# Performance work log

Hardware: AMD Instinct MI355X
Metric: run time of the kernel (lower is better)

## Reference

```python
import jax, jax.numpy as jnp
import numpy as np

BATCH = 2048
OBS_DIM = 48
H0, H1, H2 = 512, 256, 128
ACT_DIM = 12
NUM_TEACHERS = 64


def setup_inputs() -> dict:
    key = jax.random.key(0)
    ks = jax.random.split(key, 10)
    s = lambda fan_in: 1.0 / np.sqrt(fan_in)
    return {
        "obs": jax.random.normal(ks[0], (BATCH, OBS_DIM), dtype=jnp.float32),
        "teacher_indices": jax.random.randint(ks[1], (BATCH,), 0, NUM_TEACHERS),
        "w0": jax.random.normal(ks[2], (NUM_TEACHERS, H0, OBS_DIM), dtype=jnp.float32) * s(OBS_DIM),
        "b0": jax.random.normal(ks[3], (NUM_TEACHERS, H0), dtype=jnp.float32) * s(OBS_DIM),
        "w2": jax.random.normal(ks[4], (NUM_TEACHERS, H1, H0), dtype=jnp.float32) * s(H0),
        "b2": jax.random.normal(ks[5], (NUM_TEACHERS, H1), dtype=jnp.float32) * s(H0),
        "w4": jax.random.normal(ks[6], (NUM_TEACHERS, H2, H1), dtype=jnp.float32) * s(H1),
        "b4": jax.random.normal(ks[7], (NUM_TEACHERS, H2), dtype=jnp.float32) * s(H1),
        "w6": jax.random.normal(ks[8], (NUM_TEACHERS, ACT_DIM, H2), dtype=jnp.float32) * s(H2),
        "b6": jax.random.normal(ks[9], (NUM_TEACHERS, ACT_DIM), dtype=jnp.float32) * s(H2),
    }


def reference(obs, teacher_indices, w0, b0, w2, b2, w4, b4, w6, b6):
    # Per-sample gather of full teacher layer weights, then batched GEMV.
    def layer(x, w, b):
        # x: [B, in]; w[idx]: [B, out, in]; b[idx]: [B, out]
        return jnp.einsum("boi,bi->bo", w[teacher_indices], x) + b[teacher_indices]

    x = jax.nn.elu(layer(obs, w0, b0))
    x = jax.nn.elu(layer(x, w2, b2))
    x = jax.nn.elu(layer(x, w4, b4))
    x = jnp.tanh(layer(x, w6, b6))
    return x
```

## Files before the change

### kernel.cpp

```cpp
#include <hip/hip_runtime.h>

#define BATCH 2048
#define NTEACH 64

typedef __attribute__((ext_vector_type(8))) short short8;
typedef __attribute__((ext_vector_type(4))) float f32x4;

__device__ __forceinline__ unsigned short f2bf(float f) {
    unsigned u = __float_as_uint(f);
    u += 0x7FFFu + ((u >> 16) & 1u);
    return (unsigned short)(u >> 16);
}

__device__ __forceinline__ short8 cvt8(float4 a, float4 b) {
    short8 r;
    r[0] = (short)f2bf(a.x); r[1] = (short)f2bf(a.y);
    r[2] = (short)f2bf(a.z); r[3] = (short)f2bf(a.w);
    r[4] = (short)f2bf(b.x); r[5] = (short)f2bf(b.y);
    r[6] = (short)f2bf(b.z); r[7] = (short)f2bf(b.w);
    return r;
}

__device__ __forceinline__ int2 wave_scan(const int* __restrict__ tidx,
                                          int t, int* ord) {
    const int lane = threadIdx.x & 63;
    int base = 0, lt = 0;
#pragma unroll
    for (int r = 0; r < 32; ++r) {
        int i = r * 64 + lane;
        int v = tidx[i];
        bool f = (v == t);
        lt += (v < t) ? 1 : 0;
        unsigned long long b = __ballot(f);
        if (ord && f) {
            int rank = base + __builtin_popcountll(b & ((1ull << lane) - 1ull));
            ord[rank] = i;
        }
        base += __builtin_popcountll(b);
    }
#pragma unroll
    for (int off = 32; off; off >>= 1) lt += __shfl_down(lt, off);
    lt = __shfl(lt, 0);
    return make_int2(lt, base);
}

__global__ __launch_bounds__(256) void l0_kernel(const float* __restrict__ obs,
                                                 const int* __restrict__ tidx,
                                                 const float* __restrict__ w0,
                                                 const float* __restrict__ b0,
                                                 int* __restrict__ offsets_g,
                                                 int* __restrict__ order_g,
                                                 unsigned short* __restrict__ h0) {
    __shared__ int ord[BATCH];
    const int t = blockIdx.y;
    const int lane = threadIdx.x & 63, wid = threadIdx.x >> 6;
    const int ln = lane & 15, kg = lane >> 4;
    const int nq = wid & 1, mq = wid >> 1;
    const int n0 = blockIdx.x * 32 + nq * 16;

    const float* wr = w0 + ((size_t)t * 512 + n0 + ln) * 48;
    bool wvalid[2];
    float4 wa[2], wb[2];
#pragma unroll
    for (int kt = 0; kt < 2; ++kt) {
        int kb = kt * 32 + kg * 8;
        wvalid[kt] = kb < 48;
        const float* p = wr + (wvalid[kt] ? kb : 0);
        wa[kt] = *(const float4*)p;
        wb[kt] = *(const float4*)(p + 4);
    }
    const float bias = b0[(size_t)t * 512 + n0 + ln];

    int2 sc = wave_scan(tidx, t, ord);
    const int start = sc.x, count = sc.y;

    if (blockIdx.x == 0) {
        if (threadIdx.x == 0) {
            offsets_g[t] = start;
            if (t == 0) offsets_g[NTEACH] = BATCH;
        }
        for (int i = threadIdx.x; i < count; i += 256) order_g[start + i] = ord[i];
    }
    if (count == 0) return;

    short8 bf[2];
#pragma unroll
    for (int kt = 0; kt < 2; ++kt) {
        short8 z = {0, 0, 0, 0, 0, 0, 0, 0};
        bf[kt] = wvalid[kt] ? cvt8(wa[kt], wb[kt]) : z;
    }

    for (int r0 = mq * 16; r0 < count; r0 += 32) {
        int lr = r0 + ln;
        const float* xr = obs + (size_t)ord[lr < count ? lr : 0] * 48;
        short8 af[2];
#pragma unroll
        for (int kt = 0; kt < 2; ++kt) {
            int kb = kt * 32 + kg * 8;
            short8 f8 = {0, 0, 0, 0, 0, 0, 0, 0};
            if (kb < 48)
                f8 = cvt8(*(const float4*)(xr + kb), *(const float4*)(xr + kb + 4));
            af[kt] = f8;
        }
        f32x4 acc = {0.f, 0.f, 0.f, 0.f};
        acc = __builtin_amdgcn_mfma_f32_16x16x32_bf16(af[0], bf[0], acc, 0, 0, 0);
        acc = __builtin_amdgcn_mfma_f32_16x16x32_bf16(af[1], bf[1], acc, 0, 0, 0);
#pragma unroll
        for (int j = 0; j < 4; ++j) {
            int row = r0 + kg * 4 + j;
            if (row < count) {
                float v = acc[j] + bias;
                v = v > 0.f ? v : expm1f(v);
                h0[(size_t)(start + row) * 512 + n0 + ln] = f2bf(v);
            }
        }
    }
}

__global__ __launch_bounds__(256) void l1_kernel(const unsigned short* __restrict__ h0,
                                                 const int* __restrict__ offsets_g,
                                                 const float* __restrict__ w2,
                                                 const float* __restrict__ b2,
                                                 unsigned short* __restrict__ h1) {
    const int t = blockIdx.y;
    const int start = offsets_g[t];
    const int count = offsets_g[t + 1] - start;
    if (count == 0) return;
    const int lane = threadIdx.x & 63, wid = threadIdx.x >> 6;
    const int ln = lane & 15, kg = lane >> 4;
    const int nq = wid & 1, mq = wid >> 1;
    const int n0 = blockIdx.x * 32 + nq * 16;

    const float* wr = w2 + ((size_t)t * 256 + n0 + ln) * 512;
    const float bias = b2[(size_t)t * 256 + n0 + ln];
    short8 bf[16];
#pragma unroll
    for (int g = 0; g < 4; ++g) {
        float4 ta[4], tb[4];
#pragma unroll
        for (int u = 0; u < 4; ++u) {
            int kb = (g * 4 + u) * 32 + kg * 8;
            ta[u] = *(const float4*)(wr + kb);
            tb[u] = *(const float4*)(wr + kb + 4);
        }
#pragma unroll
        for (int u = 0; u < 4; ++u) bf[g * 4 + u] = cvt8(ta[u], tb[u]);
    }

    for (int r0 = mq * 16; r0 < count; r0 += 32) {
        const unsigned short* xr = h0 + (size_t)(start + r0 + ln) * 512 + kg * 8;
        f32x4 acc = {0.f, 0.f, 0.f, 0.f};
#pragma unroll
        for (int k8 = 0; k8 < 16; ++k8)
            acc = __builtin_amdgcn_mfma_f32_16x16x32_bf16(
                *(const short8*)(xr + k8 * 32), bf[k8], acc, 0, 0, 0);
#pragma unroll
        for (int j = 0; j < 4; ++j) {
            int row = r0 + kg * 4 + j;
            if (row < count) {
                float v = acc[j] + bias;
                v = v > 0.f ? v : expm1f(v);
                h1[(size_t)(start + row) * 256 + n0 + ln] = f2bf(v);
            }
        }
    }
}

__global__ __launch_bounds__(256) void l2f_kernel(const unsigned short* __restrict__ h1,
                                                  const int* __restrict__ offsets_g,
                                                  const int* __restrict__ order_g,
                                                  const float* __restrict__ w4,
                                                  const float* __restrict__ b4,
                                                  const float* __restrict__ w6,
                                                  const float* __restrict__ b6,
                                                  float* __restrict__ out) {
    __shared__ char h2b[4096];
    const int t = blockIdx.y;
    const int start = offsets_g[t];
    const int count = offsets_g[t + 1] - start;
    if ((int)blockIdx.x * 16 >= count) return;
    const int lane = threadIdx.x & 63, wid = threadIdx.x >> 6;
    const int ln = lane & 15, kg = lane >> 4;
    const int nq = wid;

    short8 bfA[2][8];
    float biasA[2];
#pragma unroll
    for (int sub = 0; sub < 2; ++sub) {
        const float* wr = w4 + ((size_t)t * 128 + nq * 32 + sub * 16 + ln) * 256;
#pragma unroll
        for (int g = 0; g < 2; ++g) {
            float4 ta[4], tb[4];
#pragma unroll
            for (int u = 0; u < 4; ++u) {
                int kb = (g * 4 + u) * 32 + kg * 8;
                ta[u] = *(const float4*)(wr + kb);
                tb[u] = *(const float4*)(wr + kb + 4);
            }
#pragma unroll
            for (int u = 0; u < 4; ++u) bfA[sub][g * 4 + u] = cvt8(ta[u], tb[u]);
        }
        biasA[sub] = b4[(size_t)t * 128 + nq * 32 + sub * 16 + ln];
    }
    short8 bf6[4];
    float bias6 = 0.f;
    if (wid == 0) {
        const float* wr = w6 + ((size_t)t * 12 + (ln < 12 ? ln : 0)) * 128;
#pragma unroll
        for (int kt = 0; kt < 4; ++kt) {
            int kb = kt * 32 + kg * 8;
            bf6[kt] = cvt8(*(const float4*)(wr + kb), *(const float4*)(wr + kb + 4));
        }
        if (ln < 12) bias6 = b6[(size_t)t * 12 + ln];
    }

    for (int mt = blockIdx.x; mt * 16 < count; mt += gridDim.x) {
        const int gr0 = start + mt * 16;
#pragma unroll
        for (int sub = 0; sub < 2; ++sub) {
            const unsigned short* xr = h1 + (size_t)(gr0 + ln) * 256 + kg * 8;
            f32x4 acc = {0.f, 0.f, 0.f, 0.f};
#pragma unroll
            for (int k8 = 0; k8 < 8; ++k8)
                acc = __builtin_amdgcn_mfma_f32_16x16x32_bf16(
                    *(const short8*)(xr + k8 * 32), bfA[sub][k8], acc, 0, 0, 0);
            int col = nq * 32 + sub * 16 + ln;
#pragma unroll
            for (int j = 0; j < 4; ++j) {
                int row = kg * 4 + j;
                float v = acc[j] + biasA[sub];
                v = v > 0.f ? v : expm1f(v);
                int byte = (row * 256 + col * 2) ^ ((row & 7) << 4);
                *(unsigned short*)(h2b + byte) = f2bf(v);
            }
        }
        __syncthreads();
        if (wid == 0) {
            f32x4 acc = {0.f, 0.f, 0.f, 0.f};
#pragma unroll
            for (int kt = 0; kt < 4; ++kt) {
                int byte = (ln * 256 + (kt * 32 + kg * 8) * 2) ^ ((ln & 7) << 4);
                acc = __builtin_amdgcn_mfma_f32_16x16x32_bf16(
                    *(const short8*)(h2b + byte), bf6[kt], acc, 0, 0, 0);
            }
#pragma unroll
            for (int j = 0; j < 4; ++j) {
                int row = mt * 16 + kg * 4 + j;
                if (ln < 12 && row < count)
                    out[(size_t)order_g[start + row] * 12 + ln] = tanhf(acc[j] + bias6);
            }
        }
        __syncthreads();
    }
}

extern "C" void kernel_launch(void* const* d_in, const int* in_sizes, int n_in,
                              void* d_out, int out_size, void* d_ws, size_t ws_size,
                              hipStream_t stream) {
    const float* obs = (const float*)d_in[0];
    const int* tidx  = (const int*)d_in[1];
    const float* w0  = (const float*)d_in[2];
    const float* b0  = (const float*)d_in[3];
    const float* w2  = (const float*)d_in[4];
    const float* b2  = (const float*)d_in[5];
    const float* w4  = (const float*)d_in[6];
    const float* b4  = (const float*)d_in[7];
    const float* w6  = (const float*)d_in[8];
    const float* b6  = (const float*)d_in[9];
    float* out = (float*)d_out;

    const int ROWS = BATCH + 16;
    char* ws = (char*)d_ws;
    int* offsets = (int*)ws;
    int* order   = (int*)(ws + 1024);
    unsigned short* h0 = (unsigned short*)(ws + 16384);
    unsigned short* h1 = h0 + (size_t)ROWS * 512;

    l0_kernel<<<dim3(16, NTEACH), 256, 0, stream>>>(obs, tidx, w0, b0,
                                                    offsets, order, h0);
    l1_kernel<<<dim3(8, NTEACH), 256, 0, stream>>>(h0, offsets, w2, b2, h1);
    l2f_kernel<<<dim3(4, NTEACH), 256, 0, stream>>>(h1, offsets, order,
                                                    w4, b4, w6, b6, out);
}
```

Measured before the change: 45.54 us.

## Fuse layers 1-3 into one kernel with split-K and last-block tail

Merges the layer-1 kernel and the layer-2/3 kernel into one launch. Layer 1 now splits K across the four waves, with an LDS reduction, over 16-column tiles, so 16 blocks per teacher share the work. The last block to finish for each teacher, found through an atomic counter reset in l0, then runs layers 2 and 3 for all of that teacher's rows in 128-row chunks. This removes a kernel launch and its gap, at the cost of serialising the tail layers onto a single block per teacher and adding a __syncthreads pair on every 16-row step of layer 1.

```diff
diff --git a/kernel.cpp b/kernel.cpp
--- a/kernel.cpp
+++ b/kernel.cpp
@@ -50,6 +50,7 @@
                                                  const float* __restrict__ b0,
                                                  int* __restrict__ offsets_g,
                                                  int* __restrict__ order_g,
+                                                 int* __restrict__ cnt_g,
                                                  unsigned short* __restrict__ h0) {
     __shared__ int ord[BATCH];
     const int t = blockIdx.y;
@@ -78,6 +79,7 @@
         if (threadIdx.x == 0) {
             offsets_g[t] = start;
             if (t == 0) offsets_g[NTEACH] = BATCH;
+            cnt_g[t] = 0;
         }
         for (int i = threadIdx.x; i < count; i += 256) order_g[start + i] = ord[i];
     }
@@ -117,135 +119,127 @@
     }
 }
 
-__global__ __launch_bounds__(256) void l1_kernel(const unsigned short* __restrict__ h0,
-                                                 const int* __restrict__ offsets_g,
-                                                 const float* __restrict__ w2,
-                                                 const float* __restrict__ b2,
-                                                 unsigned short* __restrict__ h1) {
+__global__ __launch_bounds__(256, 4) void l1f_kernel(
+    const unsigned short* __restrict__ h0, const int* __restrict__ offsets_g,
+    const int* __restrict__ order_g, int* __restrict__ cnt_g,
+    const float* __restrict__ w2, const float* __restrict__ b2,
+    const float* __restrict__ w4, const float* __restrict__ b4,
+    const float* __restrict__ w6, const float* __restrict__ b6,
+    unsigned short* __restrict__ h1, float* __restrict__ out) {
+    __shared__ f32x4 red[3][64];
+    __shared__ char h2b[32768];
+    __shared__ int done_s;
+
     const int t = blockIdx.y;
     const int start = offsets_g[t];
     const int count = offsets_g[t + 1] - start;
     if (count == 0) return;
     const int lane = threadIdx.x & 63, wid = threadIdx.x >> 6;
     const int ln = lane & 15, kg = lane >> 4;
-    const int nq = wid & 1, mq = wid >> 1;
-    const int n0 = blockIdx.x * 32 + nq * 16;
-
-    const float* wr = w2 + ((size_t)t * 256 + n0 + ln) * 512;
-    const float bias = b2[(size_t)t * 256 + n0 + ln];
-    short8 bf[16];
-#pragma unroll
-    for (int g = 0; g < 4; ++g) {
-        float4 ta[4], tb[4];
-#pragma unroll
-        for (int u = 0; u < 4; ++u) {
-            int kb = (g * 4 + u) * 32 + kg * 8;
-            ta[u] = *(const float4*)(wr + kb);
-            tb[u] = *(const float4*)(wr + kb + 4);
-        }
-#pragma unroll
-        for (int u = 0; u < 4; ++u) bf[g * 4 + u] = cvt8(ta[u], tb[u]);
-    }
-
-    for (int r0 = mq * 16; r0 < count; r0 += 32) {
-        const unsigned short* xr = h0 + (size_t)(start + r0 + ln) * 512 + kg * 8;
-        f32x4 acc = {0.f, 0.f, 0.f, 0.f};
-#pragma unroll
-        for (int k8 = 0; k8 < 16; ++k8)
-            acc = __builtin_amdgcn_mfma_f32_16x16x32_bf16(
-                *(const short8*)(xr + k8 * 32), bf[k8], acc, 0, 0, 0);
-#pragma unroll
-        for (int j = 0; j < 4; ++j) {
-            int row = r0 + kg * 4 + j;
-            if (row < count) {
-                float v = acc[j] + bias;
-                v = v > 0.f ? v : expm1f(v);
-                h1[(size_t)(start + row) * 256 + n0 + ln] = f2bf(v);
-            }
-        }
-    }
-}
-
-__global__ __launch_bounds__(256) void l2f_kernel(const unsigned short* __restrict__ h1,
-                                                  const int* __restrict__ offsets_g,
-                                                  const int* __restrict__ order_g,
-                                                  const float* __restrict__ w4,
-                                                  const float* __restrict__ b4,
-                                                  const float* __restrict__ w6,
-                                                  const float* __restrict__ b6,
-                                                  float* __restrict__ out) {
-    __shared__ char h2b[4096];
-    const int t = blockIdx.y;
-    const int start = offsets_g[t];
-    const int count = offsets_g[t + 1] - start;
-    if ((int)blockIdx.x * 16 >= count) return;
-    const int lane = threadIdx.x & 63, wid = threadIdx.x >> 6;
-    const int ln = lane & 15, kg = lane >> 4;
-    const int nq = wid;
-
-    short8 bfA[2][8];
-    float biasA[2];
-#pragma unroll
-    for (int sub = 0; sub < 2; ++sub) {
-        const float* wr = w4 + ((size_t)t * 128 + nq * 32 + sub * 16 + ln) * 256;
-#pragma unroll
-        for (int g = 0; g < 2; ++g) {
-            float4 ta[4], tb[4];
-#pragma unroll
-            for (int u = 0; u < 4; ++u) {
-                int kb = (g * 4 + u) * 32 + kg * 8;
-                ta[u] = *(const float4*)(wr + kb);
-                tb[u] = *(const float4*)(wr + kb + 4);
-            }
-#pragma unroll
-            for (int u = 0; u < 4; ++u) bfA[sub][g * 4 + u] = cvt8(ta[u], tb[u]);
-        }
-        biasA[sub] = b4[(size_t)t * 128 + nq * 32 + sub * 16 + ln];
-    }
+
+    {
+        const int n0 = blockIdx.x * 16;
+        const int kbase = wid * 128;
+        short8 bf[4];
+        const float* wr = w2 + ((size_t)t * 256 + n0 + ln) * 512 + kbase;
+#pragma unroll
+        for (int k8 = 0; k8 < 4; ++k8) {
+            int kb = k8 * 32 + kg * 8;
+            bf[k8] = cvt8(*(const float4*)(wr + kb), *(const float4*)(wr + kb + 4));
+        }
+        const float bias = b2[(size_t)t * 256 + n0 + ln];
+        for (int r0 = 0; r0 < count; r0 += 16) {
+            const unsigned short* xr =
+                h0 + (size_t)(start + r0 + ln) * 512 + kbase + kg * 8;
+            f32x4 acc = {0.f, 0.f, 0.f, 0.f};
+#pragma unroll
+            for (int k8 = 0; k8 < 4; ++k8)
+                acc = __builtin_amdgcn_mfma_f32_16x16x32_bf16(
+                    *(const short8*)(xr + k8 * 32), bf[k8], acc, 0, 0, 0);
+            __syncthreads();
+            if (wid > 0) red[wid - 1][lane] = acc;
+            __syncthreads();
+            if (wid == 0) {
+#pragma unroll
+                for (int s = 0; s < 3; ++s) {
+                    f32x4 r = red[s][lane];
+                    acc[0] += r[0]; acc[1] += r[1]; acc[2] += r[2]; acc[3] += r[3];
+                }
+#pragma unroll
+                for (int j = 0; j < 4; ++j) {
+                    int row = r0 + kg * 4 + j;
+                    if (row < count) {
+                        float v = acc[j] + bias;
+                        v = v > 0.f ? v : expm1f(v);
+                        h1[(size_t)(start + row) * 256 + n0 + ln] = f2bf(v);
+                    }
+                }
+            }
+        }
+    }
+
+    __threadfence();
+    if (threadIdx.x == 0) done_s = atomicAdd(&cnt_g[t], 1);
+    __syncthreads();
+    if (done_s != 15) return;
+    __threadfence();
+
     short8 bf6[4];
-    float bias6 = 0.f;
-    if (wid == 0) {
+    {
         const float* wr = w6 + ((size_t)t * 12 + (ln < 12 ? ln : 0)) * 128;
 #pragma unroll
         for (int kt = 0; kt < 4; ++kt) {
             int kb = kt * 32 + kg * 8;
             bf6[kt] = cvt8(*(const float4*)(wr + kb), *(const float4*)(wr + kb + 4));
         }
-        if (ln < 12) bias6 = b6[(size_t)t * 12 + ln];
-    }
-
-    for (int mt = blockIdx.x; mt * 16 < count; mt += gridDim.x) {
-        const int gr0 = start + mt * 16;
+    }
+    const float bias6 = (ln < 12) ? b6[(size_t)t * 12 + ln] : 0.f;
+    const int n0q = wid * 32;
+
+    for (int sc0 = 0; sc0 < count; sc0 += 128) {
+        const int lim = min(count - sc0, 128);
 #pragma unroll
         for (int sub = 0; sub < 2; ++sub) {
-            const unsigned short* xr = h1 + (size_t)(gr0 + ln) * 256 + kg * 8;
+            const int col = n0q + sub * 16 + ln;
+            short8 bfH[8];
+            const float* wr = w4 + ((size_t)t * 128 + col) * 256;
+#pragma unroll
+            for (int k8 = 0; k8 < 8; ++k8) {
+                int kb = k8 * 32 + kg * 8;
+                bfH[k8] = cvt8(*(const float4*)(wr + kb), *(const float4*)(wr + kb + 4));
+            }
+            const float biasH = b4[(size_t)t * 128 + col];
+            for (int c0 = 0; c0 < lim; c0 += 16) {
+                const unsigned short* xr =
+                    h1 + (size_t)(start + sc0 + c0 + ln) * 256 + kg * 8;
+                f32x4 acc = {0.f, 0.f, 0.f, 0.f};
+#pragma unroll
+                for (int k8 = 0; k8 < 8; ++k8)
+                    acc = __builtin_amdgcn_mfma_f32_16x16x32_bf16(
+                        *(const short8*)(xr + k8 * 32), bfH[k8], acc, 0, 0, 0);
+#pragma unroll
+                for (int j = 0; j < 4; ++j) {
+                    int rr = c0 + kg * 4 + j;
+                    float v = acc[j] + biasH;
+                    v = v > 0.f ? v : expm1f(v);
+                    int byte = (rr * 256 + col * 2) ^ ((rr & 7) << 4);
+                    *(unsigned short*)(h2b + byte) = f2bf(v);
+                }
+            }
+        }
+        __syncthreads();
+        for (int c0 = wid * 16; c0 < lim; c0 += 64) {
             f32x4 acc = {0.f, 0.f, 0.f, 0.f};
-#pragma unroll
-            for (int k8 = 0; k8 < 8; ++k8)
-                acc = __builtin_amdgcn_mfma_f32_16x16x32_bf16(
-                    *(const short8*)(xr + k8 * 32), bfA[sub][k8], acc, 0, 0, 0);
-            int col = nq * 32 + sub * 16 + ln;
-#pragma unroll
-            for (int j = 0; j < 4; ++j) {
-                int row = kg * 4 + j;
-                float v = acc[j] + biasA[sub];
-                v = v > 0.f ? v : expm1f(v);
-                int byte = (row * 256 + col * 2) ^ ((row & 7) << 4);
-                *(unsigned short*)(h2b + byte) = f2bf(v);
-            }
-        }
-        __syncthreads();
-        if (wid == 0) {
-            f32x4 acc = {0.f, 0.f, 0.f, 0.f};
+            int rr = c0 + ln;
 #pragma unroll
             for (int kt = 0; kt < 4; ++kt) {
-                int byte = (ln * 256 + (kt * 32 + kg * 8) * 2) ^ ((ln & 7) << 4);
+                int byte = (rr * 256 + (kt * 32 + kg * 8) * 2) ^ ((rr & 7) << 4);
                 acc = __builtin_amdgcn_mfma_f32_16x16x32_bf16(
                     *(const short8*)(h2b + byte), bf6[kt], acc, 0, 0, 0);
             }
 #pragma unroll
             for (int j = 0; j < 4; ++j) {
-                int row = mt * 16 + kg * 4 + j;
+                int row = sc0 + c0 + kg * 4 + j;
                 if (ln < 12 && row < count)
                     out[(size_t)order_g[start + row] * 12 + ln] = tanhf(acc[j] + bias6);
             }
@@ -272,13 +266,14 @@
     const int ROWS = BATCH + 16;
     char* ws = (char*)d_ws;
     int* offsets = (int*)ws;
+    int* cnt     = (int*)(ws + 512);
     int* order   = (int*)(ws + 1024);
     unsigned short* h0 = (unsigned short*)(ws + 16384);
     unsigned short* h1 = h0 + (size_t)ROWS * 512;
 
     l0_kernel<<<dim3(16, NTEACH), 256, 0, stream>>>(obs, tidx, w0, b0,
-                                                    offsets, order, h0);
-    l1_kernel<<<dim3(8, NTEACH), 256, 0, stream>>>(h0, offsets, w2, b2, h1);
-    l2f_kernel<<<dim3(4, NTEACH), 256, 0, stream>>>(h1, offsets, order,
-                                                    w4, b4, w6, b6, out);
-}
+                                                    offsets, order, cnt, h0);
+    l1f_kernel<<<dim3(16, NTEACH), 256, 0, stream>>>(h0, offsets, order, cnt,
+                                                     w2, b2, w4, b4, w6, b6,
+                                                     h1, out);
+}
```

Result: slower. 170.5 us (+274.3%).

## Split l1 reduction dimension across waves with LDS reduce, double l1 grid

Applied to the files above, without the earlier changes.

The layer-1 kernel now assigns each of the four waves a quarter of the K dimension for a 16-column tile instead of splitting by N and M, then reduces partial accumulators through shared memory. The grid doubles to 16 column tiles per teacher, giving each thread fewer weight registers and more blocks in flight. In exchange it adds two block barriers per 16-row tile and serializes the epilogue on one wave. The l2f kernel also hoists its activation loads out of the sub loop so both sub-tiles reuse the same registers.

```diff
diff --git a/kernel.cpp b/kernel.cpp
--- a/kernel.cpp
+++ b/kernel.cpp
@@ -122,45 +122,50 @@
                                                  const float* __restrict__ w2,
                                                  const float* __restrict__ b2,
                                                  unsigned short* __restrict__ h1) {
+    __shared__ f32x4 red[3][64];
     const int t = blockIdx.y;
     const int start = offsets_g[t];
     const int count = offsets_g[t + 1] - start;
     if (count == 0) return;
     const int lane = threadIdx.x & 63, wid = threadIdx.x >> 6;
     const int ln = lane & 15, kg = lane >> 4;
-    const int nq = wid & 1, mq = wid >> 1;
-    const int n0 = blockIdx.x * 32 + nq * 16;
-
-    const float* wr = w2 + ((size_t)t * 256 + n0 + ln) * 512;
+    const int n0 = blockIdx.x * 16;
+    const int kbase = wid * 128;
+
+    short8 bf[4];
+    const float* wr = w2 + ((size_t)t * 256 + n0 + ln) * 512 + kbase;
+#pragma unroll
+    for (int k8 = 0; k8 < 4; ++k8) {
+        int kb = k8 * 32 + kg * 8;
+        bf[k8] = cvt8(*(const float4*)(wr + kb), *(const float4*)(wr + kb + 4));
+    }
     const float bias = b2[(size_t)t * 256 + n0 + ln];
-    short8 bf[16];
-#pragma unroll
-    for (int g = 0; g < 4; ++g) {
-        float4 ta[4], tb[4];
-#pragma unroll
-        for (int u = 0; u < 4; ++u) {
-            int kb = (g * 4 + u) * 32 + kg * 8;
-            ta[u] = *(const float4*)(wr + kb);
-            tb[u] = *(const float4*)(wr + kb + 4);
-        }
-#pragma unroll
-        for (int u = 0; u < 4; ++u) bf[g * 4 + u] = cvt8(ta[u], tb[u]);
-    }
-
-    for (int r0 = mq * 16; r0 < count; r0 += 32) {
-        const unsigned short* xr = h0 + (size_t)(start + r0 + ln) * 512 + kg * 8;
+
+    for (int r0 = 0; r0 < count; r0 += 16) {
+        const unsigned short* xr =
+            h0 + (size_t)(start + r0 + ln) * 512 + kbase + kg * 8;
         f32x4 acc = {0.f, 0.f, 0.f, 0.f};
 #pragma unroll
-        for (int k8 = 0; k8 < 16; ++k8)
+        for (int k8 = 0; k8 < 4; ++k8)
             acc = __builtin_amdgcn_mfma_f32_16x16x32_bf16(
                 *(const short8*)(xr + k8 * 32), bf[k8], acc, 0, 0, 0);
-#pragma unroll
-        for (int j = 0; j < 4; ++j) {
-            int row = r0 + kg * 4 + j;
-            if (row < count) {
-                float v = acc[j] + bias;
-                v = v > 0.f ? v : expm1f(v);
-                h1[(size_t)(start + row) * 256 + n0 + ln] = f2bf(v);
+        __syncthreads();
+        if (wid > 0) red[wid - 1][lane] = acc;
+        __syncthreads();
+        if (wid == 0) {
+#pragma unroll
+            for (int s = 0; s < 3; ++s) {
+                f32x4 r = red[s][lane];
+                acc[0] += r[0]; acc[1] += r[1]; acc[2] += r[2]; acc[3] += r[3];
+            }
+#pragma unroll
+            for (int j = 0; j < 4; ++j) {
+                int row = r0 + kg * 4 + j;
+                if (row < count) {
+                    float v = acc[j] + bias;
+                    v = v > 0.f ? v : expm1f(v);
+                    h1[(size_t)(start + row) * 256 + n0 + ln] = f2bf(v);
+                }
             }
         }
     }
@@ -189,16 +194,9 @@
     for (int sub = 0; sub < 2; ++sub) {
         const float* wr = w4 + ((size_t)t * 128 + nq * 32 + sub * 16 + ln) * 256;
 #pragma unroll
-        for (int g = 0; g < 2; ++g) {
-            float4 ta[4], tb[4];
-#pragma unroll
-            for (int u = 0; u < 4; ++u) {
-                int kb = (g * 4 + u) * 32 + kg * 8;
-                ta[u] = *(const float4*)(wr + kb);
-                tb[u] = *(const float4*)(wr + kb + 4);
-            }
-#pragma unroll
-            for (int u = 0; u < 4; ++u) bfA[sub][g * 4 + u] = cvt8(ta[u], tb[u]);
+        for (int k8 = 0; k8 < 8; ++k8) {
+            int kb = k8 * 32 + kg * 8;
+            bfA[sub][k8] = cvt8(*(const float4*)(wr + kb), *(const float4*)(wr + kb + 4));
         }
         biasA[sub] = b4[(size_t)t * 128 + nq * 32 + sub * 16 + ln];
     }
@@ -216,14 +214,17 @@
 
     for (int mt = blockIdx.x; mt * 16 < count; mt += gridDim.x) {
         const int gr0 = start + mt * 16;
+        short8 af[8];
+        const unsigned short* xr = h1 + (size_t)(gr0 + ln) * 256 + kg * 8;
+#pragma unroll
+        for (int k8 = 0; k8 < 8; ++k8) af[k8] = *(const short8*)(xr + k8 * 32);
 #pragma unroll
         for (int sub = 0; sub < 2; ++sub) {
-            const unsigned short* xr = h1 + (size_t)(gr0 + ln) * 256 + kg * 8;
             f32x4 acc = {0.f, 0.f, 0.f, 0.f};
 #pragma unroll
             for (int k8 = 0; k8 < 8; ++k8)
-                acc = __builtin_amdgcn_mfma_f32_16x16x32_bf16(
-                    *(const short8*)(xr + k8 * 32), bfA[sub][k8], acc, 0, 0, 0);
+                acc = __builtin_amdgcn_mfma_f32_16x16x32_bf16(af[k8], bfA[sub][k8],
+                                                              acc, 0, 0, 0);
             int col = nq * 32 + sub * 16 + ln;
 #pragma unroll
             for (int j = 0; j < 4; ++j) {
@@ -278,7 +279,7 @@
 
     l0_kernel<<<dim3(16, NTEACH), 256, 0, stream>>>(obs, tidx, w0, b0,
                                                     offsets, order, h0);
-    l1_kernel<<<dim3(8, NTEACH), 256, 0, stream>>>(h0, offsets, w2, b2, h1);
+    l1_kernel<<<dim3(16, NTEACH), 256, 0, stream>>>(h0, offsets, w2, b2, h1);
     l2f_kernel<<<dim3(4, NTEACH), 256, 0, stream>>>(h1, offsets, order,
                                                     w4, b4, w6, b6, out);
 }
```

Result: faster. 42.79 us (-6.1%).
